# Kernel tuning notes

Measured on AMD Instinct MI355X. Metric: run time of the kernel, lower is better.

## Reference

```python
import jax, jax.numpy as jnp
import numpy as np

B, C, H, W = 4, 384, 64, 64
NH = 8
HD = C // NH
SR = 2
SCALE = HD ** -0.5
Hs, Ws = H // SR, W // SR
NK = Hs * Ws


def setup_inputs() -> dict:
    key = jax.random.key(0)
    ks = jax.random.split(key, 8)
    s = 0.02
    return {
        "x": jax.random.normal(ks[0], (B, C, H, W), jnp.float32),
        "Wq": jax.random.normal(ks[1], (C, C), jnp.float32) * s,
        "Wk": jax.random.normal(ks[2], (C, C), jnp.float32) * s,
        "Wv": jax.random.normal(ks[3], (C, C), jnp.float32) * s,
        "Wsr": jax.random.normal(ks[4], (C, C, SR, SR), jnp.float32) * s,
        "bsr": jnp.zeros((C,), jnp.float32),
        "Wp": jax.random.normal(ks[5], (C, C), jnp.float32) * s,
        "bp": jnp.zeros((C,), jnp.float32),
        "rel_h": jax.random.normal(ks[6], (1, NH, HD, 1, Hs), jnp.float32),
        "rel_w": jax.random.normal(ks[7], (1, NH, HD, Ws, 1), jnp.float32),
    }


def _mhsa(x, Wq, Wk, Wv, Wsr, bsr, Wp, bp, rel_h, rel_w):
    Bq = x.shape[0]
    # 1x1 conv == channel matmul
    q = jnp.einsum('oc,bchw->bohw', Wq, x).reshape(Bq, NH, HD, H * W)
    # spatial reduction: Conv2d(kernel=SR, stride=SR); norm defaults to Identity
    xsr = jax.lax.conv_general_dilated(
        x, Wsr, window_strides=(SR, SR), padding='VALID',
        dimension_numbers=('NCHW', 'OIHW', 'NCHW')) + bsr[None, :, None, None]
    k = jnp.einsum('oc,bchw->bohw', Wk, xsr).reshape(Bq, NH, HD, NK)
    v = jnp.einsum('oc,bchw->bohw', Wv, xsr).reshape(Bq, NH, HD, NK)
    # relative positional bias fused into keys
    pos = (rel_h + rel_w).reshape(1, NH, HD, NK)
    k = (k + pos) * SCALE
    # attn[b,h,n,m] = q^T k, softmax over keys (dropout is identity at p=0)
    attn = jax.nn.softmax(jnp.einsum('bhdn,bhdm->bhnm', q, k), axis=-1)
    out = jnp.einsum('bhdm,bhnm->bhdn', v, attn).reshape(Bq, C, H, W)
    out = jnp.einsum('oc,bchw->bohw', Wp, out) + bp[None, :, None, None]
    return out


def reference(x, Wq, Wk, Wv, Wsr, bsr, Wp, bp, rel_h, rel_w):
    return _mhsa(x, Wq, Wk, Wv, Wsr, bsr, Wp, bp, rel_h, rel_w)
```

## Files before the change

kernel.cpp:

```cpp
#include <hip/hip_runtime.h>
#include <hip/hip_bf16.h>
#include <math.h>

typedef __attribute__((ext_vector_type(8))) short b16x8;
typedef __attribute__((ext_vector_type(4))) short b16x4;
typedef __attribute__((ext_vector_type(4))) float floatx4;
typedef __attribute__((ext_vector_type(16))) float f32x16;

constexpr int BATCH = 4, CCH = 384, NQ = 4096, NHD = 8, HDIM = 48, NK = 1024;
constexpr float SCALE = 0.14433756729740643f;
constexpr float SCALE_L2E = 0.14433756729740643f * 1.4426950408889634f;

__device__ inline unsigned short f2bf(float f) {
    unsigned u = __builtin_bit_cast(unsigned, f);
    u += 0x7fffu + ((u >> 16) & 1u);
    return (unsigned short)(u >> 16);
}

__device__ __forceinline__ void g2lds16(const void* g, void* l) {
    __builtin_amdgcn_global_load_lds(
        (const __attribute__((address_space(1))) unsigned int*)g,
        (__attribute__((address_space(3))) unsigned int*)l, 16, 0, 0);
}

__global__ void cvt_all(const float* __restrict__ Wq, const float* __restrict__ Wk,
                        const float* __restrict__ Wv, const float* __restrict__ Wsr,
                        const float* __restrict__ Wp, const float* __restrict__ bsr,
                        short* __restrict__ WqB, short* __restrict__ WkvB,
                        short* __restrict__ WsrT, short* __restrict__ WpB,
                        float* __restrict__ kvb) {
    int job = blockIdx.y;
    if (job == 3) {
        for (int j = blockIdx.x * 256 + threadIdx.x; j < 589824; j += gridDim.x * 256) {
            int kin = j / 384, o = j - kin * 384;
            int p = kin / 384, cin = kin - p * 384;
            WsrT[j] = (short)f2bf(Wsr[o * 1536 + cin * 4 + p]);
        }
        return;
    }
    if (job == 5) {
        int o2 = blockIdx.x * 256 + threadIdx.x;
        if (o2 < 768) {
            const float* wrow = (o2 < 384) ? (Wk + (size_t)o2 * 384)
                                           : (Wv + (size_t)(o2 - 384) * 384);
            float ssum = 0.f;
            for (int c = 0; c < 384; c++) ssum += wrow[c] * bsr[c];
            kvb[o2] = ssum;
        }
        return;
    }
    const float* src; short* dst;
    if (job == 0)      { src = Wq;  dst = WqB; }
    else if (job == 1) { src = Wk;  dst = WkvB; }
    else if (job == 2) { src = Wv;  dst = WkvB + 147456; }
    else               { src = Wp;  dst = WpB; }
    for (int i = blockIdx.x * 256 + threadIdx.x; i < 147456; i += gridDim.x * 256)
        dst[i] = (short)f2bf(src[i]);
}

__global__ void t1_kern(const float* __restrict__ x, short* __restrict__ xT) {
    int b = blockIdx.z, s = blockIdx.x * 64 + (threadIdx.x & 63);
    for (int c8 = blockIdx.y * 8 + (threadIdx.x >> 6); c8 < blockIdx.y * 8 + 8; c8 += 4) {
        b16x8 pk;
        #pragma unroll
        for (int e = 0; e < 8; e++)
            pk[e] = (short)f2bf(x[((size_t)b * CCH + c8 * 8 + e) * NQ + s]);
        *(b16x8*)(xT + ((size_t)b * NQ + s) * CCH + c8 * 8) = pk;
    }
}

__global__ __launch_bounds__(256, 2) void combine_gemm(
    const short* __restrict__ WsrT, const short* __restrict__ WkvB,
    short* __restrict__ Wc)
{
    __shared__ short At[128 * 64];
    __shared__ short Bt[128 * 64];
    const int o0 = blockIdx.y * 128, s0 = blockIdx.x * 128;
    const int t = threadIdx.x, wave = t >> 6, lane = t & 63, g = lane >> 4, li = lane & 15;
    const int wr = wave >> 1, wc = wave & 1;
    floatx4 acc[4][4] = {};

    for (int k0 = 0; k0 < 384; k0 += 64) {
        __syncthreads();
        #pragma unroll
        for (int it = 0; it < 4; it++) {
            int task = it * 256 + t;
            int row = task >> 3, ch = task & 7;
            int cont = ch ^ (row & 7);
            g2lds16(WsrT + (size_t)(o0 + row) * 384 + k0 + cont * 8, At + task * 8);
        }
        #pragma unroll
        for (int it = 0; it < 4; it++) {
            int task = it * 256 + t;
            int row = task >> 3, ch = task & 7;
            int cont = ch ^ (row & 7);
            g2lds16(WkvB + (size_t)(s0 + row) * 384 + k0 + cont * 8, Bt + task * 8);
        }
        __syncthreads();
        #pragma unroll
        for (int kk = 0; kk < 2; kk++) {
            b16x8 af[4], bf[4];
            #pragma unroll
            for (int mi = 0; mi < 4; mi++) {
                int r = wr * 64 + mi * 16 + li;
                af[mi] = *(const b16x8*)(At + r * 64 + (((kk * 4 + g) ^ (r & 7)) * 8));
            }
            #pragma unroll
            for (int nf = 0; nf < 4; nf++) {
                int r = wc * 64 + nf * 16 + li;
                bf[nf] = *(const b16x8*)(Bt + r * 64 + (((kk * 4 + g) ^ (r & 7)) * 8));
            }
            #pragma unroll
            for (int mi = 0; mi < 4; mi++)
                #pragma unroll
                for (int nf = 0; nf < 4; nf++)
                    acc[mi][nf] = __builtin_amdgcn_mfma_f32_16x16x32_bf16(af[mi], bf[nf], acc[mi][nf], 0, 0, 0);
        }
    }

    #pragma unroll
    for (int mi = 0; mi < 4; mi++) {
        #pragma unroll
        for (int nf = 0; nf < 4; nf++) {
            int o = o0 + wr * 64 + mi * 16 + g * 4;
            int s = s0 + wc * 64 + nf * 16 + li;
            b16x4 pk;
            #pragma unroll
            for (int j = 0; j < 4; j++) pk[j] = (short)f2bf(acc[mi][nf][j]);
            *(b16x4*)(Wc + (size_t)s * 1536 + o) = pk;
        }
    }
}

__global__ __launch_bounds__(256, 2) void fused_qkv(
    const short* __restrict__ WqB, const short* __restrict__ Wc,
    const short* __restrict__ xT, const float* __restrict__ kvb,
    const float* __restrict__ relh, const float* __restrict__ relw,
    short* __restrict__ qTb, short* __restrict__ kTb, short* __restrict__ vCb)
{
    __shared__ short At[128 * 64];
    __shared__ short Bt[128 * 64];
    const int b = blockIdx.z;
    const int id = blockIdx.x;
    const bool kv = id >= 96;
    const int sx = kv ? ((id - 96) & 7) : (id & 31);
    const int oy = kv ? ((id - 96) >> 3) : (id >> 5);
    const int Ks = kv ? 1536 : 384;
    const short* A = kv ? Wc : WqB;
    const int o0 = oy * 128, s0 = sx * 128;
    const int t = threadIdx.x, wave = t >> 6, lane = t & 63, g = lane >> 4, li = lane & 15;
    const int wr = wave >> 1, wc = wave & 1;
    floatx4 acc[4][4] = {};
    const short* Bbase = xT + (size_t)b * NQ * CCH;

    for (int k0 = 0; k0 < Ks; k0 += 64) {
        __syncthreads();
        #pragma unroll
        for (int it = 0; it < 4; it++) {
            int task = it * 256 + t;
            int row = task >> 3, ch = task & 7;
            int cont = ch ^ (row & 7);
            g2lds16(A + (size_t)(o0 + row) * Ks + k0 + cont * 8, At + task * 8);
        }
        #pragma unroll
        for (int it = 0; it < 4; it++) {
            int task = it * 256 + t;
            int row = task >> 3, ch = task & 7;
            int cont = ch ^ (row & 7);
            if (kv) {
                int ssr = s0 + row;
                int hs = ssr >> 5, wsv = ssr & 31;
                int k = k0 + cont * 8;
                int p = k / 384, coff = k - p * 384;
                g2lds16(Bbase + (size_t)((2 * hs + (p >> 1)) * 64 + 2 * wsv + (p & 1)) * 384 + coff,
                        Bt + task * 8);
            } else {
                g2lds16(Bbase + (size_t)(s0 + row) * 384 + k0 + cont * 8, Bt + task * 8);
            }
        }
        __syncthreads();
        #pragma unroll
        for (int kk = 0; kk < 2; kk++) {
            b16x8 af[4], bf[4];
            #pragma unroll
            for (int mi = 0; mi < 4; mi++) {
                int r = wr * 64 + mi * 16 + li;
                af[mi] = *(const b16x8*)(At + r * 64 + (((kk * 4 + g) ^ (r & 7)) * 8));
            }
            #pragma unroll
            for (int nf = 0; nf < 4; nf++) {
                int r = wc * 64 + nf * 16 + li;
                bf[nf] = *(const b16x8*)(Bt + r * 64 + (((kk * 4 + g) ^ (r & 7)) * 8));
            }
            #pragma unroll
            for (int mi = 0; mi < 4; mi++)
                #pragma unroll
                for (int nf = 0; nf < 4; nf++)
                    acc[mi][nf] = __builtin_amdgcn_mfma_f32_16x16x32_bf16(af[mi], bf[nf], acc[mi][nf], 0, 0, 0);
        }
    }

    #pragma unroll
    for (int mi = 0; mi < 4; mi++) {
        #pragma unroll
        for (int nf = 0; nf < 4; nf++) {
            int o = o0 + wr * 64 + mi * 16 + g * 4;
            int s = s0 + wc * 64 + nf * 16 + li;
            if (!kv) {
                b16x4 pk;
                #pragma unroll
                for (int j = 0; j < 4; j++) pk[j] = (short)f2bf(acc[mi][nf][j]);
                *(b16x4*)(qTb + ((size_t)b * NQ + s) * CCH + o) = pk;
            } else if (o0 < 384) {
                int hs = s >> 5, wsv = s & 31;
                b16x4 pk;
                #pragma unroll
                for (int j = 0; j < 4; j++)
                    pk[j] = (short)f2bf((acc[mi][nf][j] + kvb[o + j]
                                         + relh[(o + j) * 32 + wsv]
                                         + relw[(o + j) * 32 + hs]) * SCALE_L2E);
                *(b16x4*)(kTb + ((size_t)b * NK + s) * CCH + o) = pk;
            } else {
                #pragma unroll
                for (int j = 0; j < 4; j++)
                    vCb[((size_t)b * CCH + (o - 384 + j)) * NK + s] =
                        (short)f2bf(acc[mi][nf][j] + kvb[o + j]);
            }
        }
    }
}

__global__ __launch_bounds__(256, 2) void p_gemm(
    const short* __restrict__ A, const short* __restrict__ Bm,
    float* __restrict__ Yf, const float* __restrict__ bias)
{
    __shared__ short At[128 * 64];
    __shared__ short Bt[128 * 64];
    const int b = blockIdx.z, o0 = blockIdx.y * 128, s0 = blockIdx.x * 128;
    const int t = threadIdx.x, wave = t >> 6, lane = t & 63, g = lane >> 4, li = lane & 15;
    const int wr = wave >> 1, wc = wave & 1;
    floatx4 acc[4][4] = {};
    const short* Bbase = Bm + (size_t)b * NQ * CCH;

    for (int k0 = 0; k0 < 384; k0 += 64) {
        __syncthreads();
        #pragma unroll
        for (int it = 0; it < 4; it++) {
            int task = it * 256 + t;
            int row = task >> 3, ch = task & 7;
            int cont = ch ^ (row & 7);
            g2lds16(A + (size_t)(o0 + row) * 384 + k0 + cont * 8, At + task * 8);
        }
        #pragma unroll
        for (int it = 0; it < 4; it++) {
            int task = it * 256 + t;
            int row = task >> 3, ch = task & 7;
            int cont = ch ^ (row & 7);
            g2lds16(Bbase + (size_t)(s0 + row) * 384 + k0 + cont * 8, Bt + task * 8);
        }
        __syncthreads();
        #pragma unroll
        for (int kk = 0; kk < 2; kk++) {
            b16x8 af[4], bf[4];
            #pragma unroll
            for (int mi = 0; mi < 4; mi++) {
                int r = wr * 64 + mi * 16 + li;
                af[mi] = *(const b16x8*)(At + r * 64 + (((kk * 4 + g) ^ (r & 7)) * 8));
            }
            #pragma unroll
            for (int nf = 0; nf < 4; nf++) {
                int r = wc * 64 + nf * 16 + li;
                bf[nf] = *(const b16x8*)(Bt + r * 64 + (((kk * 4 + g) ^ (r & 7)) * 8));
            }
            #pragma unroll
            for (int mi = 0; mi < 4; mi++)
                #pragma unroll
                for (int nf = 0; nf < 4; nf++)
                    acc[mi][nf] = __builtin_amdgcn_mfma_f32_16x16x32_bf16(af[mi], bf[nf], acc[mi][nf], 0, 0, 0);
        }
    }

    #pragma unroll
    for (int mi = 0; mi < 4; mi++) {
        #pragma unroll
        for (int nf = 0; nf < 4; nf++) {
            int o = o0 + wr * 64 + mi * 16 + g * 4;
            int s = s0 + wc * 64 + nf * 16 + li;
            #pragma unroll
            for (int j = 0; j < 4; j++)
                Yf[((size_t)b * CCH + o + j) * (size_t)NQ + s] = acc[mi][nf][j] + bias[o + j];
        }
    }
}

__global__ __launch_bounds__(256, 4) void attn_kern(
    const short* __restrict__ qT, const short* __restrict__ kT,
    const short* __restrict__ vC, short* __restrict__ attT)
{
    __shared__ short Kl[2][6 * 64 * 8];
    __shared__ short Vl[2][8 * 64 * 8];
    const int wgid = blockIdx.x;
    const int nid = (wgid & 7) * 128 + (wgid >> 3);
    const int qt = nid & 31, hh = (nid >> 5) & 7, b = nid >> 8;
    const int t = threadIdx.x, wave = t >> 6, lane = t & 63;
    const int h = lane >> 5, c = lane & 31;
    const int n0 = qt * 128 + wave * 32;

    const short* qp = qT + (size_t)b * NQ * CCH + hh * HDIM;
    const short* kp = kT + (size_t)b * NK * CCH + hh * HDIM;
    const short* vp = vC + ((size_t)b * CCH + hh * HDIM) * NK;

    {
        int bufi = t >> 7, rem = t & 127;
        int ch = rem >> 4, row = 48 + (rem & 15);
        b16x8 val = {};
        if (row == 48)
            #pragma unroll
            for (int e = 0; e < 8; e++) val[e] = (short)0x3F80;
        *(b16x8*)(&Vl[bufi][(ch * 64 + row) * 8]) = val;
    }

    b16x8 qf[3];
    #pragma unroll
    for (int dc = 0; dc < 3; dc++)
        qf[dc] = *(const b16x8*)(qp + (size_t)(n0 + c) * CCH + dc * 16 + h * 8);

    auto stage = [&](int m0, int bi) {
        #pragma unroll
        for (int it = 0; it < 2; it++) {
            int task = it * 256 + wave * 64 + lane;
            int ch = task >> 6, row = task & 63;
            if (ch < 6) {
                int key = (row & 51) | ((row & 4) << 1) | ((row & 8) >> 1);
                g2lds16(kp + (size_t)(m0 + key) * CCH + ch * 8, &Kl[bi][task * 8]);
            }
        }
        #pragma unroll
        for (int it = 0; it < 2; it++) {
            int task = it * 256 + wave * 64 + lane;
            int ch = task >> 6, row = task & 63;
            if (row < 48)
                g2lds16(vp + (size_t)row * NK + m0 + ch * 8, &Vl[bi][task * 8]);
        }
    };

    f32x16 O[2] = {};

    stage(0, 0);
    for (int tt = 0; tt < 16; ++tt) {
        __syncthreads();
        if (tt < 15) stage((tt + 1) * 64, (tt + 1) & 1);
        const short* Kb = Kl[tt & 1];
        const short* Vb = Vl[tt & 1];
        #pragma unroll
        for (int kb = 0; kb < 2; kb++) {
            b16x8 kf[3];
            #pragma unroll
            for (int dc = 0; dc < 3; dc++)
                kf[dc] = *(const b16x8*)(Kb + (((dc * 2 + h) * 64) + kb * 32 + c) * 8);
            f32x16 s = {};
            __builtin_amdgcn_s_setprio(1);
            #pragma unroll
            for (int dc = 0; dc < 3; dc++)
                s = __builtin_amdgcn_mfma_f32_32x32x16_bf16(kf[dc], qf[dc], s, 0, 0, 0);
            __builtin_amdgcn_s_setprio(0);
            float p[16];
            #pragma unroll
            for (int r = 0; r < 16; r++)
                p[r] = __builtin_amdgcn_exp2f(s[r]);
            b16x8 pfrag[2];
            #pragma unroll
            for (int kk = 0; kk < 2; kk++) {
                union { unsigned u[4]; b16x8 v; } w;
                #pragma unroll
                for (int wd = 0; wd < 4; wd++)
                    asm("v_cvt_pk_bf16_f32 %0, %1, %2"
                        : "=v"(w.u[wd])
                        : "v"(p[kk * 8 + wd * 2]), "v"(p[kk * 8 + wd * 2 + 1]));
                pfrag[kk] = w.v;
            }
            __builtin_amdgcn_s_setprio(1);
            #pragma unroll
            for (int kk = 0; kk < 2; kk++)
                #pragma unroll
                for (int db = 0; db < 2; db++) {
                    b16x8 vf = *(const b16x8*)(Vb + (((kb * 4 + kk * 2 + h) * 64) + db * 32 + c) * 8);
                    O[db] = __builtin_amdgcn_mfma_f32_32x32x16_bf16(pfrag[kk], vf, O[db], 0, 0, 0);
                }
            __builtin_amdgcn_s_setprio(0);
        }
    }

    __syncthreads();
    short* Olw = ((short*)Vl) + wave * 2048;
    #pragma unroll
    for (int r = 0; r < 16; r++) {
        int qrow = (r & 3) + 8 * (r >> 2) + 4 * h;
        float lr = __shfl(O[1][r], (lane & 32) | 16);
        float iq = 1.0f / lr;
        #pragma unroll
        for (int db = 0; db < 2; db++) {
            int d = db * 32 + c;
            if (d < 48)
                Olw[qrow * 64 + (((d >> 3) ^ (qrow & 7)) * 8) + (d & 7)] =
                    (short)f2bf(O[db][r] * iq);
        }
    }
    __syncthreads();
    #pragma unroll
    for (int it = 0; it < 4; it++) {
        int idx = it * 64 + lane;
        int row = idx >> 3, c8 = idx & 7;
        if (c8 < 6) {
            b16x8 val = *(const b16x8*)(Olw + row * 64 + ((c8 ^ (row & 7)) * 8));
            *(b16x8*)(attT + ((size_t)b * NQ + n0 + row) * CCH + hh * HDIM + c8 * 8) = val;
        }
    }
}

extern "C" void kernel_launch(void* const* d_in, const int* in_sizes, int n_in,
                              void* d_out, int out_size, void* d_ws, size_t ws_size,
                              hipStream_t stream) {
    const float* x    = (const float*)d_in[0];
    const float* Wq   = (const float*)d_in[1];
    const float* Wk   = (const float*)d_in[2];
    const float* Wv   = (const float*)d_in[3];
    const float* Wsr  = (const float*)d_in[4];
    const float* bsr  = (const float*)d_in[5];
    const float* Wp   = (const float*)d_in[6];
    const float* bp   = (const float*)d_in[7];
    const float* relh = (const float*)d_in[8];
    const float* relw = (const float*)d_in[9];
    float* out = (float*)d_out;

    short* ws = (short*)d_ws;
    size_t off = 0;
    auto alloc = [&](size_t n) { short* p = ws + off; off += n; return p; };
    short* WqB  = alloc(147456);
    short* WkvB = alloc(294912);
    short* WsrT = alloc(589824);
    short* WpB  = alloc(147456);
    short* WcB  = alloc(768 * 1536);
    short* kvbh = alloc(768 * 2);
    short* xT   = alloc((size_t)BATCH * NQ * CCH);
    short* qTb  = alloc((size_t)BATCH * NQ * CCH);
    short* kTb  = alloc((size_t)BATCH * NK * CCH);
    short* vCb  = alloc((size_t)BATCH * CCH * NK);
    short* attT = alloc((size_t)BATCH * NQ * CCH);
    float* kvb  = (float*)kvbh;

    cvt_all<<<dim3(576, 6), 256, 0, stream>>>(Wq, Wk, Wv, Wsr, Wp, bsr,
                                              WqB, WkvB, WsrT, WpB, kvb);
    combine_gemm<<<dim3(6, 12), 256, 0, stream>>>(WsrT, WkvB, WcB);
    t1_kern<<<dim3(64, 6, BATCH), 256, 0, stream>>>(x, xT);
    fused_qkv<<<dim3(144, 1, BATCH), 256, 0, stream>>>(
        WqB, WcB, xT, kvb, relh, relw, qTb, kTb, vCb);
    attn_kern<<<dim3(1024), 256, 0, stream>>>(qTb, kTb, vCb, attT);
    p_gemm<<<dim3(32, 3, BATCH), 256, 0, stream>>>(WpB, attT, out, bp);
}
```

Measured before the change: 126.1 us.

## Double query rows per attention wave and fold x transpose into prep kernel

Each attention wave now handles two 32-row query blocks, so the K/V tiles staged in LDS and each K fragment serve twice as many queries. The grid is halved to 512 workgroups and launch bounds are dropped to 2 blocks per CU to make room for the extra registers. Staging address math is hoisted out of the loop. The separate x transpose/convert kernel is merged into the weight-prep kernel as a seventh job, removing one launch. The trade-off is lower occupancy and fewer workgroups, roughly two per CU on a 256-CU part, which may leave latency less well hidden.

```diff
diff --git a/kernel.cpp b/kernel.cpp
--- a/kernel.cpp
+++ b/kernel.cpp
@@ -23,13 +23,28 @@
         (__attribute__((address_space(3))) unsigned int*)l, 16, 0, 0);
 }
 
-__global__ void cvt_all(const float* __restrict__ Wq, const float* __restrict__ Wk,
-                        const float* __restrict__ Wv, const float* __restrict__ Wsr,
-                        const float* __restrict__ Wp, const float* __restrict__ bsr,
-                        short* __restrict__ WqB, short* __restrict__ WkvB,
-                        short* __restrict__ WsrT, short* __restrict__ WpB,
-                        float* __restrict__ kvb) {
+__global__ void prep_kern(const float* __restrict__ Wq, const float* __restrict__ Wk,
+                          const float* __restrict__ Wv, const float* __restrict__ Wsr,
+                          const float* __restrict__ Wp, const float* __restrict__ bsr,
+                          const float* __restrict__ x,
+                          short* __restrict__ WqB, short* __restrict__ WkvB,
+                          short* __restrict__ WsrT, short* __restrict__ WpB,
+                          float* __restrict__ kvb, short* __restrict__ xT) {
     int job = blockIdx.y;
+    if (job == 6) {
+        for (int i = blockIdx.x * 256 + threadIdx.x; i < BATCH * 4096 * 48;
+             i += 576 * 256) {
+            int b = i / (4096 * 48);
+            int rem = i - b * (4096 * 48);
+            int c8 = rem / 4096, s = rem - c8 * 4096;
+            b16x8 pk;
+            #pragma unroll
+            for (int e = 0; e < 8; e++)
+                pk[e] = (short)f2bf(x[((size_t)b * CCH + c8 * 8 + e) * NQ + s]);
+            *(b16x8*)(xT + ((size_t)b * NQ + s) * CCH + c8 * 8) = pk;
+        }
+        return;
+    }
     if (job == 3) {
         for (int j = blockIdx.x * 256 + threadIdx.x; j < 589824; j += gridDim.x * 256) {
             int kin = j / 384, o = j - kin * 384;
@@ -56,17 +71,6 @@
     else               { src = Wp;  dst = WpB; }
     for (int i = blockIdx.x * 256 + threadIdx.x; i < 147456; i += gridDim.x * 256)
         dst[i] = (short)f2bf(src[i]);
-}
-
-__global__ void t1_kern(const float* __restrict__ x, short* __restrict__ xT) {
-    int b = blockIdx.z, s = blockIdx.x * 64 + (threadIdx.x & 63);
-    for (int c8 = blockIdx.y * 8 + (threadIdx.x >> 6); c8 < blockIdx.y * 8 + 8; c8 += 4) {
-        b16x8 pk;
-        #pragma unroll
-        for (int e = 0; e < 8; e++)
-            pk[e] = (short)f2bf(x[((size_t)b * CCH + c8 * 8 + e) * NQ + s]);
-        *(b16x8*)(xT + ((size_t)b * NQ + s) * CCH + c8 * 8) = pk;
-    }
 }
 
 __global__ __launch_bounds__(256, 2) void combine_gemm(
@@ -293,18 +297,18 @@
     }
 }
 
-__global__ __launch_bounds__(256, 4) void attn_kern(
+__global__ __launch_bounds__(256, 2) void attn_kern(
     const short* __restrict__ qT, const short* __restrict__ kT,
     const short* __restrict__ vC, short* __restrict__ attT)
 {
     __shared__ short Kl[2][6 * 64 * 8];
     __shared__ short Vl[2][8 * 64 * 8];
     const int wgid = blockIdx.x;
-    const int nid = (wgid & 7) * 128 + (wgid >> 3);
-    const int qt = nid & 31, hh = (nid >> 5) & 7, b = nid >> 8;
+    const int nid = (wgid & 7) * 64 + (wgid >> 3);
+    const int qt = nid & 15, hh = (nid >> 4) & 7, b = nid >> 7;
     const int t = threadIdx.x, wave = t >> 6, lane = t & 63;
     const int h = lane >> 5, c = lane & 31;
-    const int n0 = qt * 128 + wave * 32;
+    const int n0 = qt * 256 + wave * 64;
 
     const short* qp = qT + (size_t)b * NQ * CCH + hh * HDIM;
     const short* kp = kT + (size_t)b * NK * CCH + hh * HDIM;
@@ -320,31 +324,33 @@
         *(b16x8*)(&Vl[bufi][(ch * 64 + row) * 8]) = val;
     }
 
-    b16x8 qf[3];
+    b16x8 qf[2][3];
     #pragma unroll
-    for (int dc = 0; dc < 3; dc++)
-        qf[dc] = *(const b16x8*)(qp + (size_t)(n0 + c) * CCH + dc * 16 + h * 8);
+    for (int qb = 0; qb < 2; qb++)
+        #pragma unroll
+        for (int dc = 0; dc < 3; dc++)
+            qf[qb][dc] = *(const b16x8*)(qp + (size_t)(n0 + qb * 32 + c) * CCH + dc * 16 + h * 8);
+
+    const int rowS = t & 63;
+    const int chA = t >> 6;
+    const int keyS = (rowS & 51) | ((rowS & 4) << 1) | ((rowS & 8) >> 1);
+    const short* ksrcA = kp + (size_t)keyS * CCH + chA * 8;
+    const bool  kvalB = (chA + 4) < 6;
+    const bool  vval  = rowS < 48;
+    const short* vsrcA = vp + (size_t)rowS * NK + chA * 8;
+    const int taskA8 = t * 8, taskB8 = (t + 256) * 8;
 
     auto stage = [&](int m0, int bi) {
-        #pragma unroll
-        for (int it = 0; it < 2; it++) {
-            int task = it * 256 + wave * 64 + lane;
-            int ch = task >> 6, row = task & 63;
-            if (ch < 6) {
-                int key = (row & 51) | ((row & 4) << 1) | ((row & 8) >> 1);
-                g2lds16(kp + (size_t)(m0 + key) * CCH + ch * 8, &Kl[bi][task * 8]);
-            }
-        }
-        #pragma unroll
-        for (int it = 0; it < 2; it++) {
-            int task = it * 256 + wave * 64 + lane;
-            int ch = task >> 6, row = task & 63;
-            if (row < 48)
-                g2lds16(vp + (size_t)row * NK + m0 + ch * 8, &Vl[bi][task * 8]);
+        size_t koff = (size_t)m0 * CCH;
+        g2lds16(ksrcA + koff, &Kl[bi][taskA8]);
+        if (kvalB) g2lds16(ksrcA + koff + 32, &Kl[bi][taskB8]);
+        if (vval) {
+            g2lds16(vsrcA + m0, &Vl[bi][taskA8]);
+            g2lds16(vsrcA + m0 + 32, &Vl[bi][taskB8]);
         }
     };
 
-    f32x16 O[2] = {};
+    f32x16 O[2][2] = {};
 
     stage(0, 0);
     for (int tt = 0; tt < 16; ++tt) {
@@ -358,26 +364,31 @@
             #pragma unroll
             for (int dc = 0; dc < 3; dc++)
                 kf[dc] = *(const b16x8*)(Kb + (((dc * 2 + h) * 64) + kb * 32 + c) * 8);
-            f32x16 s = {};
+            f32x16 s0v = {}, s1v = {};
             __builtin_amdgcn_s_setprio(1);
             #pragma unroll
-            for (int dc = 0; dc < 3; dc++)
-                s = __builtin_amdgcn_mfma_f32_32x32x16_bf16(kf[dc], qf[dc], s, 0, 0, 0);
+            for (int dc = 0; dc < 3; dc++) {
+                s0v = __builtin_amdgcn_mfma_f32_32x32x16_bf16(kf[dc], qf[0][dc], s0v, 0, 0, 0);
+                s1v = __builtin_amdgcn_mfma_f32_32x32x16_bf16(kf[dc], qf[1][dc], s1v, 0, 0, 0);
+            }
             __builtin_amdgcn_s_setprio(0);
-            float p[16];
-            #pragma unroll
-            for (int r = 0; r < 16; r++)
-                p[r] = __builtin_amdgcn_exp2f(s[r]);
-            b16x8 pfrag[2];
-            #pragma unroll
-            for (int kk = 0; kk < 2; kk++) {
-                union { unsigned u[4]; b16x8 v; } w;
-                #pragma unroll
-                for (int wd = 0; wd < 4; wd++)
-                    asm("v_cvt_pk_bf16_f32 %0, %1, %2"
-                        : "=v"(w.u[wd])
-                        : "v"(p[kk * 8 + wd * 2]), "v"(p[kk * 8 + wd * 2 + 1]));
-                pfrag[kk] = w.v;
+            b16x8 pfrag[2][2];
+            #pragma unroll
+            for (int qb = 0; qb < 2; qb++) {
+                float p[16];
+                #pragma unroll
+                for (int r = 0; r < 16; r++)
+                    p[r] = __builtin_amdgcn_exp2f(qb ? s1v[r] : s0v[r]);
+                #pragma unroll
+                for (int kk = 0; kk < 2; kk++) {
+                    union { unsigned u[4]; b16x8 v; } w;
+                    #pragma unroll
+                    for (int wd = 0; wd < 4; wd++)
+                        asm("v_cvt_pk_bf16_f32 %0, %1, %2"
+                            : "=v"(w.u[wd])
+                            : "v"(p[kk * 8 + wd * 2]), "v"(p[kk * 8 + wd * 2 + 1]));
+                    pfrag[qb][kk] = w.v;
+                }
             }
             __builtin_amdgcn_s_setprio(1);
             #pragma unroll
@@ -385,7 +396,9 @@
                 #pragma unroll
                 for (int db = 0; db < 2; db++) {
                     b16x8 vf = *(const b16x8*)(Vb + (((kb * 4 + kk * 2 + h) * 64) + db * 32 + c) * 8);
-                    O[db] = __builtin_amdgcn_mfma_f32_32x32x16_bf16(pfrag[kk], vf, O[db], 0, 0, 0);
+                    #pragma unroll
+                    for (int qb = 0; qb < 2; qb++)
+                        O[qb][db] = __builtin_amdgcn_mfma_f32_32x32x16_bf16(pfrag[qb][kk], vf, O[qb][db], 0, 0, 0);
                 }
             __builtin_amdgcn_s_setprio(0);
         }
@@ -394,26 +407,28 @@
     __syncthreads();
     short* Olw = ((short*)Vl) + wave * 2048;
     #pragma unroll
-    for (int r = 0; r < 16; r++) {
-        int qrow = (r & 3) + 8 * (r >> 2) + 4 * h;
-        float lr = __shfl(O[1][r], (lane & 32) | 16);
-        float iq = 1.0f / lr;
-        #pragma unroll
-        for (int db = 0; db < 2; db++) {
-            int d = db * 32 + c;
-            if (d < 48)
-                Olw[qrow * 64 + (((d >> 3) ^ (qrow & 7)) * 8) + (d & 7)] =
-                    (short)f2bf(O[db][r] * iq);
-        }
-    }
-    __syncthreads();
-    #pragma unroll
-    for (int it = 0; it < 4; it++) {
-        int idx = it * 64 + lane;
-        int row = idx >> 3, c8 = idx & 7;
-        if (c8 < 6) {
-            b16x8 val = *(const b16x8*)(Olw + row * 64 + ((c8 ^ (row & 7)) * 8));
-            *(b16x8*)(attT + ((size_t)b * NQ + n0 + row) * CCH + hh * HDIM + c8 * 8) = val;
+    for (int qb = 0; qb < 2; qb++) {
+        #pragma unroll
+        for (int r = 0; r < 16; r++) {
+            int qrow = (r & 3) + 8 * (r >> 2) + 4 * h;
+            float lr = __shfl(O[qb][1][r], (lane & 32) | 16);
+            float iq = 1.0f / lr;
+            #pragma unroll
+            for (int db = 0; db < 2; db++) {
+                int d = db * 32 + c;
+                if (d < 48)
+                    Olw[qrow * 64 + (((d >> 3) ^ (qrow & 7)) * 8) + (d & 7)] =
+                        (short)f2bf(O[qb][db][r] * iq);
+            }
+        }
+        #pragma unroll
+        for (int it = 0; it < 4; it++) {
+            int idx = it * 64 + lane;
+            int row = idx >> 3, c8 = idx & 7;
+            if (c8 < 6) {
+                b16x8 val = *(const b16x8*)(Olw + row * 64 + ((c8 ^ (row & 7)) * 8));
+                *(b16x8*)(attT + ((size_t)b * NQ + n0 + qb * 32 + row) * CCH + hh * HDIM + c8 * 8) = val;
+            }
         }
     }
 }
@@ -449,12 +464,11 @@
     short* attT = alloc((size_t)BATCH * NQ * CCH);
     float* kvb  = (float*)kvbh;
 
-    cvt_all<<<dim3(576, 6), 256, 0, stream>>>(Wq, Wk, Wv, Wsr, Wp, bsr,
-                                              WqB, WkvB, WsrT, WpB, kvb);
+    prep_kern<<<dim3(576, 7), 256, 0, stream>>>(Wq, Wk, Wv, Wsr, Wp, bsr, x,
+                                                WqB, WkvB, WsrT, WpB, kvb, xT);
     combine_gemm<<<dim3(6, 12), 256, 0, stream>>>(WsrT, WkvB, WcB);
-    t1_kern<<<dim3(64, 6, BATCH), 256, 0, stream>>>(x, xT);
     fused_qkv<<<dim3(144, 1, BATCH), 256, 0, stream>>>(
         WqB, WcB, xT, kvb, relh, relw, qTb, kTb, vCb);
-    attn_kern<<<dim3(1024), 256, 0, stream>>>(qTb, kTb, vCb, attT);
+    attn_kern<<<dim3(512), 256, 0, stream>>>(qTb, kTb, vCb, attT);
     p_gemm<<<dim3(32, 3, BATCH), 256, 0, stream>>>(WpB, attT, out, bp);
 }
```

Result: faster. 122.6 us (-2.8%).
